# Performance work log

Measured on AMD Instinct MI355X. Metric: run time of the kernel, lower is better.

Reference implementation:

```python
import jax, jax.numpy as jnp
import numpy as np

MAX_ATOMS = 14  # hard-coded padded atom slots per residue in the original module


def setup_inputs() -> dict:
    key = jax.random.key(0)
    k1, k2, k3 = jax.random.split(key, 3)
    N_RES = 100000
    C = 128  # config.m; OutputLayer(3) emits m channels, fc1 = Linear(14*m, 1)
    feature = jax.random.normal(k1, (N_RES * MAX_ATOMS, C), dtype=jnp.float32)
    atom_num = jax.random.randint(k2, (N_RES,), 0, MAX_ATOMS, dtype=jnp.int32)
    label_binary = jax.random.randint(k3, (N_RES,), 0, 2, dtype=jnp.int32)
    return {"feature": feature, "atom_num": atom_num, "label_binary": label_binary}


def reference(feature, atom_num, label_binary):
    # Ragged gather-to-padded: atoms of residue r live at flat positions
    # [offset[r], offset[r]+atom_num[r]) in `feature`; copy into slot [r, :atom_num[r], :]
    # of a zero-padded [N_res, 14, C] tensor (the original nested Python loop).
    counts = atom_num.astype(jnp.int32)
    offsets = jnp.concatenate([jnp.zeros((1,), jnp.int32), jnp.cumsum(counts)[:-1]])  # [N_res]
    slots = jnp.arange(MAX_ATOMS, dtype=jnp.int32)                                    # [14]
    idx = offsets[:, None] + slots[None, :]                                           # [N_res, 14]
    mask = slots[None, :] < counts[:, None]                                           # [N_res, 14]
    idx = jnp.clip(idx, 0, feature.shape[0] - 1)
    padded = feature[idx] * mask[:, :, None].astype(feature.dtype)                    # [N_res, 14, C]
    aa_feature = padded.reshape(padded.shape[0], -1)                                  # [N_res, 14*C]
    return aa_feature, label_binary
```

## Files before the change

### kernel.cpp

```cpp
#include <hip/hip_runtime.h>


#define MAX_ATOMS 14
#define F4_PER_ROW 32
#define F4_PER_RES (MAX_ATOMS * F4_PER_ROW)
#define TILE 16
#define GBLOCKS 512
#define GTHREADS 1024

typedef float f32x4 __attribute__((ext_vector_type(4)));

__global__ __launch_bounds__(256) void k_sums(const int* __restrict__ atom_num,
                                              int n, int* __restrict__ sums) {
    __shared__ int lds[256];
    int t = threadIdx.x;
    int r = blockIdx.x * 256 + t;
    lds[t] = (r < n) ? atom_num[r] : 0;
    __syncthreads();
    for (int d = 128; d > 0; d >>= 1) {
        if (t < d) lds[t] += lds[t + d];
        __syncthreads();
    }
    if (t == 0) sums[blockIdx.x] = lds[0];
}

__global__ __launch_bounds__(256) void k_prep(const int* __restrict__ atom_num,
                                              const int* __restrict__ sums,
                                              const int* __restrict__ label,
                                              int n,
                                              int* __restrict__ offsets,
                                              float* __restrict__ out_label) {
    __shared__ int red[256];
    __shared__ int scn[256];
    int t = threadIdx.x;
    int b = blockIdx.x;
    int part = 0;
    for (int j = t; j < b; j += 256) part += sums[j];
    red[t] = part;
    __syncthreads();
    for (int d = 128; d > 0; d >>= 1) {
        if (t < d) red[t] += red[t + d];
        __syncthreads();
    }
    int base = red[0];
    int r = b * 256 + t;
    int v = (r < n) ? atom_num[r] : 0;
    scn[t] = v;
    __syncthreads();
    for (int d = 1; d < 256; d <<= 1) {
        int add = (t >= d) ? scn[t - d] : 0;
        __syncthreads();
        scn[t] += add;
        __syncthreads();
    }
    if (r < n) {
        offsets[r] = base + scn[t] - v;
        out_label[r] = (float)label[r];
    }
}

__global__ __launch_bounds__(GTHREADS, 8) void k_gather(
        const f32x4* __restrict__ feat,
        const int* __restrict__ atom_num,
        const int* __restrict__ offsets,
        f32x4* __restrict__ out,
        int n, int ntiles) {
    int w       = threadIdx.x >> 6;
    int lane    = threadIdx.x & 63;
    int halfrow = lane >> 5;

    for (int tile = blockIdx.x; tile < ntiles; tile += GBLOCKS) {
        int r = tile * TILE + w;
        if (r < n) {
            int off = offsets[r];
            int cnt = atom_num[r];
            const f32x4* fp = feat + (size_t)off * F4_PER_ROW + lane;
            f32x4* op = out + (size_t)r * F4_PER_RES + lane;
            #pragma unroll
            for (int i = 0; i < 7; ++i) {
                f32x4 v = (f32x4)0.f;
                if (2 * i + halfrow < cnt)
                    v = __builtin_nontemporal_load(fp + i * 64);
                op[i * 64] = v;
            }
        }
    }
}

extern "C" void kernel_launch(void* const* d_in, const int* in_sizes, int n_in,
                              void* d_out, int out_size, void* d_ws, size_t ws_size,
                              hipStream_t stream) {
    const float* feature = (const float*)d_in[0];
    const int* atom_num  = (const int*)d_in[1];
    const int* label     = (const int*)d_in[2];
    const int n = in_sizes[1];

    float* out = (float*)d_out;
    float* out_label = out + (size_t)n * MAX_ATOMS * 128;

    int nb = (n + 255) / 256;
    int* ws_sums    = (int*)d_ws;
    int* ws_offsets = ws_sums + nb;

    k_sums<<<nb, 256, 0, stream>>>(atom_num, n, ws_sums);
    k_prep<<<nb, 256, 0, stream>>>(atom_num, ws_sums, label, n,
                                   ws_offsets, out_label);

    int ntiles = (n + TILE - 1) / TILE;
    k_gather<<<GBLOCKS, GTHREADS, 0, stream>>>(
        (const f32x4*)feature, atom_num, ws_offsets,
        (f32x4*)out, n, ntiles);
}
```

Before: 215.3 us.

## Fuse scan and gather into one cooperative kernel with grid sync

Replaces the three launches (block sums, prefix scan, gather) with a single cooperative kernel. Each of 512 blocks scans its chunk of residues, publishes its block total, and after a grid sync adds the prefix of the earlier blocks before a second grid sync and the gather. Output stores also become nontemporal. This removes two launch gaps and intermediate passes, at the cost of grid-wide barriers and a requirement that rpb fit within 1024 threads, which holds for n=100000.

```diff
diff --git a/kernel.cpp b/kernel.cpp
--- a/kernel.cpp
+++ b/kernel.cpp
@@ -1,4 +1,7 @@
 #include <hip/hip_runtime.h>
+#include <hip/hip_cooperative_groups.h>
+
+namespace cg = cooperative_groups;
 
 
 #define MAX_ATOMS 14
@@ -10,78 +13,64 @@
 
 typedef float f32x4 __attribute__((ext_vector_type(4)));
 
-__global__ __launch_bounds__(256) void k_sums(const int* __restrict__ atom_num,
-                                              int n, int* __restrict__ sums) {
-    __shared__ int lds[256];
-    int t = threadIdx.x;
-    int r = blockIdx.x * 256 + t;
-    lds[t] = (r < n) ? atom_num[r] : 0;
-    __syncthreads();
-    for (int d = 128; d > 0; d >>= 1) {
-        if (t < d) lds[t] += lds[t + d];
-        __syncthreads();
-    }
-    if (t == 0) sums[blockIdx.x] = lds[0];
-}
-
-__global__ __launch_bounds__(256) void k_prep(const int* __restrict__ atom_num,
-                                              const int* __restrict__ sums,
-                                              const int* __restrict__ label,
-                                              int n,
-                                              int* __restrict__ offsets,
-                                              float* __restrict__ out_label) {
-    __shared__ int red[256];
-    __shared__ int scn[256];
+__global__ __launch_bounds__(GTHREADS, 8) void k_fused(
+        const f32x4* __restrict__ feat,
+        const int* __restrict__ atom_num,
+        const int* __restrict__ label,
+        f32x4* __restrict__ out,
+        float* __restrict__ out_label,
+        int* __restrict__ ws_off,
+        int* __restrict__ ws_sums,
+        int n, int ntiles, int rpb) {
+    cg::grid_group grid = cg::this_grid();
+    __shared__ int scn[GTHREADS];
     int t = threadIdx.x;
     int b = blockIdx.x;
-    int part = 0;
-    for (int j = t; j < b; j += 256) part += sums[j];
-    red[t] = part;
-    __syncthreads();
-    for (int d = 128; d > 0; d >>= 1) {
-        if (t < d) red[t] += red[t + d];
-        __syncthreads();
-    }
-    int base = red[0];
-    int r = b * 256 + t;
-    int v = (r < n) ? atom_num[r] : 0;
+
+    int r = b * rpb + t;
+    int v = (t < rpb && r < n) ? atom_num[r] : 0;
     scn[t] = v;
     __syncthreads();
-    for (int d = 1; d < 256; d <<= 1) {
+    for (int d = 1; d < GTHREADS; d <<= 1) {
         int add = (t >= d) ? scn[t - d] : 0;
         __syncthreads();
         scn[t] += add;
         __syncthreads();
     }
-    if (r < n) {
-        offsets[r] = base + scn[t] - v;
+    if (t < rpb && r < n) {
+        ws_off[r] = scn[t] - v;
         out_label[r] = (float)label[r];
     }
-}
+    if (t == GTHREADS - 1) ws_sums[b] = scn[t];
+    grid.sync();
 
-__global__ __launch_bounds__(GTHREADS, 8) void k_gather(
-        const f32x4* __restrict__ feat,
-        const int* __restrict__ atom_num,
-        const int* __restrict__ offsets,
-        f32x4* __restrict__ out,
-        int n, int ntiles) {
-    int w       = threadIdx.x >> 6;
-    int lane    = threadIdx.x & 63;
+    scn[t] = (t < b) ? ws_sums[t] : 0;
+    __syncthreads();
+    for (int d = GTHREADS / 2; d > 0; d >>= 1) {
+        if (t < d) scn[t] += scn[t + d];
+        __syncthreads();
+    }
+    int base = scn[0];
+    if (t < rpb && r < n) ws_off[r] += base;
+    grid.sync();
+
+    int w       = t >> 6;
+    int lane    = t & 63;
     int halfrow = lane >> 5;
 
-    for (int tile = blockIdx.x; tile < ntiles; tile += GBLOCKS) {
-        int r = tile * TILE + w;
-        if (r < n) {
-            int off = offsets[r];
-            int cnt = atom_num[r];
+    for (int tile = b; tile < ntiles; tile += GBLOCKS) {
+        int rr = tile * TILE + w;
+        if (rr < n) {
+            int off = ws_off[rr];
+            int cnt = atom_num[rr];
             const f32x4* fp = feat + (size_t)off * F4_PER_ROW + lane;
-            f32x4* op = out + (size_t)r * F4_PER_RES + lane;
+            f32x4* op = out + (size_t)rr * F4_PER_RES + lane;
             #pragma unroll
             for (int i = 0; i < 7; ++i) {
-                f32x4 v = (f32x4)0.f;
+                f32x4 vv = (f32x4)0.f;
                 if (2 * i + halfrow < cnt)
-                    v = __builtin_nontemporal_load(fp + i * 64);
-                op[i * 64] = v;
+                    vv = __builtin_nontemporal_load(fp + i * 64);
+                __builtin_nontemporal_store(vv, op + i * 64);
             }
         }
     }
@@ -90,24 +79,25 @@
 extern "C" void kernel_launch(void* const* d_in, const int* in_sizes, int n_in,
                               void* d_out, int out_size, void* d_ws, size_t ws_size,
                               hipStream_t stream) {
-    const float* feature = (const float*)d_in[0];
+    const f32x4* feature = (const f32x4*)d_in[0];
     const int* atom_num  = (const int*)d_in[1];
     const int* label     = (const int*)d_in[2];
-    const int n = in_sizes[1];
+    int n = in_sizes[1];
 
-    float* out = (float*)d_out;
-    float* out_label = out + (size_t)n * MAX_ATOMS * 128;
+    f32x4* out = (f32x4*)d_out;
+    float* out_label = (float*)d_out + (size_t)n * MAX_ATOMS * 128;
 
-    int nb = (n + 255) / 256;
-    int* ws_sums    = (int*)d_ws;
-    int* ws_offsets = ws_sums + nb;
-
-    k_sums<<<nb, 256, 0, stream>>>(atom_num, n, ws_sums);
-    k_prep<<<nb, 256, 0, stream>>>(atom_num, ws_sums, label, n,
-                                   ws_offsets, out_label);
+    int* ws_off  = (int*)d_ws;
+    int* ws_sums = ws_off + n;
 
     int ntiles = (n + TILE - 1) / TILE;
-    k_gather<<<GBLOCKS, GTHREADS, 0, stream>>>(
-        (const f32x4*)feature, atom_num, ws_offsets,
-        (f32x4*)out, n, ntiles);
+    int rpb = (n + GBLOCKS - 1) / GBLOCKS;
+
+    void* args[] = { (void*)&feature, (void*)&atom_num, (void*)&label,
+                     (void*)&out, (void*)&out_label,
+                     (void*)&ws_off, (void*)&ws_sums,
+                     (void*)&n, (void*)&ntiles, (void*)&rpb };
+    hipLaunchCooperativeKernel((const void*)k_fused,
+                               dim3(GBLOCKS), dim3(GTHREADS),
+                               args, 0, stream);
 }
```

Measured after the change: 309.1 us. +43.6%, slower.
